# Optimization experiments

Hardware: AMD Instinct MI355X
Metric: run time of the kernel (lower is better)

Reference implementation:

```python
import jax, jax.numpy as jnp
import numpy as np

TAU = 2.0        # config.init_tau
VTH = 1.0        # config.v_threshold
KS = 25          # dilated_kernel_size == config.max_delay
EPS = 1e-5       # BatchNorm eps
ALPHA = 2.0      # atan surrogate alpha (spikingjelly default)

B, C_IN, C_INH, C_OUT, T, KC = 128, 512, 256, 512, 512, 1


def dcls_kernel(W, P, SIG):
    """Dcls1d 'gauss' version: build dense kernel [O, I, KS] by Gaussian
    interpolation of kernel_count weights at learnable positions P with
    spread SIG.  W, P, SIG: [O, I, KC]."""
    grid = jnp.arange(KS, dtype=W.dtype)                      # [KS]
    g = jnp.exp(-0.5 * ((grid - P[..., None]) / SIG[..., None]) ** 2)  # [O,I,KC,KS]
    g = g / (g.sum(-1, keepdims=True) + 1e-7)
    return jnp.einsum('oik,oikd->oid', W, g)                  # [O, I, KS]


def causal_conv1d(x, K):
    # x: [B, Cin, T], K: [Cout, Cin, KS] -> [B, Cout, T], left (causal) padding
    return jax.lax.conv_general_dilated(
        x, K, window_strides=(1,), padding=[(KS - 1, 0)],
        dimension_numbers=('NCH', 'OIH', 'NCH'))


@jax.custom_vjp
def spike_fn(v):
    return (v >= 0.0).astype(v.dtype)

def _spike_fwd(v):
    return spike_fn(v), v

def _spike_bwd(v, g):
    # atan surrogate gradient
    return (g * (ALPHA / 2.0) / (1.0 + (jnp.pi / 2.0 * ALPHA * v) ** 2),)

spike_fn.defvjp(_spike_fwd, _spike_bwd)


def lif_multistep(h):
    # h: [B, C, T] -> spikes [B, C, T]; decay_input=False, hard reset to 0,
    # detach_reset=True (stop_gradient on reset path)
    hT = jnp.transpose(h, (2, 0, 1))                          # [T, B, C]

    def step(v, h_t):
        v = v - v / TAU + h_t
        s = spike_fn(v - VTH)
        v = v * (1.0 - jax.lax.stop_gradient(s))
        return v, s

    v0 = jnp.zeros(hT.shape[1:], hT.dtype)
    _, sT = jax.lax.scan(step, v0, hT)
    return jnp.transpose(sT, (1, 2, 0))                       # [B, C, T]


def setup_inputs() -> dict:
    key = jax.random.key(0)
    ks = jax.random.split(key, 12)
    f = jnp.float32

    def w(k, o, i):
        return jax.random.uniform(k, (o, i, KC), dtype=f) / np.sqrt(i * KS)

    def p(k, o, i):
        return jax.random.uniform(k, (o, i, KC), dtype=f) * (KS - 1)

    return {
        'x': jax.random.normal(ks[0], (B, C_IN, T), dtype=f),
        'W_ie': w(ks[1], C_INH, C_IN), 'P_ie': p(ks[2], C_INH, C_IN),
        'SIG_ie': jnp.full((C_INH, C_IN, KC), 0.5, dtype=f),
        'W_oi': w(ks[3], C_OUT, C_INH), 'P_oi': p(ks[4], C_OUT, C_INH),
        'SIG_oi': jnp.full((C_OUT, C_INH, KC), 0.5, dtype=f),
        'W_ee': w(ks[5], C_OUT, C_IN), 'P_ee': p(ks[6], C_OUT, C_IN),
        'SIG_ee': jnp.full((C_OUT, C_IN, KC), 0.5, dtype=f),
        'bn_gamma': jnp.ones((C_INH,), dtype=f),
        'bn_beta': jnp.zeros((C_INH,), dtype=f),
        'bias': jax.random.uniform(ks[7], (C_OUT,), dtype=f,
                                   minval=-1.0, maxval=1.0) / np.sqrt(C_IN),
    }


def reference(x, W_ie, P_ie, SIG_ie, W_oi, P_oi, SIG_oi,
              W_ee, P_ee, SIG_ee, bn_gamma, bn_beta, bias):
    # input -> inhibitory (Dale positive weights)
    K_ie = dcls_kernel(jnp.abs(W_ie), P_ie, SIG_ie)
    h = causal_conv1d(x, K_ie)                                # [B, C_INH, T]

    # multi-step BatchNorm1d (training stats over batch and time)
    mean = h.mean((0, 2), keepdims=True)
    var = h.var((0, 2), keepdims=True)
    h = (h - mean) * jax.lax.rsqrt(var + EPS)
    h = h * bn_gamma[None, :, None] + bn_beta[None, :, None]

    # LIF spiking recurrence over time
    s = lif_multistep(h)                                      # [B, C_INH, T]

    # inhibitory -> output (Dale negative), input -> output (Dale positive)
    K_oi = dcls_kernel(-jnp.abs(W_oi), P_oi, SIG_oi)
    K_ee = dcls_kernel(jnp.abs(W_ee), P_ee, SIG_ee)
    out = causal_conv1d(s, K_oi) + causal_conv1d(x, K_ee)
    out = out + bias[None, :, None]
    return out
```

## Files before the change

### kernel.cpp

```cpp
#include <hip/hip_runtime.h>
#include <stdint.h>

#define B_    128
#define T_    512
#define PT_   536
#define CIN_  512
#define CINH_ 256
#define COUT_ 512
#define KS25  25

typedef __attribute__((ext_vector_type(8))) short s16x8;
typedef __attribute__((ext_vector_type(4))) float f32x4;

typedef const __attribute__((address_space(1))) void gas_t;
typedef __attribute__((address_space(3))) void las_t;

__device__ __forceinline__ short f2bf(float f) {
    union { float f; uint32_t u; } v; v.f = f;
    uint32_t r = v.u + 0x7fffu + ((v.u >> 16) & 1u);
    return (short)(r >> 16);
}
__device__ __forceinline__ float bf2f(short s) {
    union { uint32_t u; float f; } v; v.u = ((uint32_t)(uint16_t)s) << 16;
    return v.f;
}

__device__ __forceinline__ void gload16(const void* g, void* l) {
    __builtin_amdgcn_global_load_lds((gas_t*)g, (las_t*)l, 16, 0, 0);
}

template<int NCHUNK>
__device__ __forceinline__ void stage_tile(const short* src, short* lds, int stride, int tid) {
    const int wbase = tid & ~63;
    #pragma unroll
    for (int c = 0; c < (NCHUNK + 255) / 256; ++c) {
        int idx = c * 256 + tid;
        if ((NCHUNK % 256 == 0) || idx < NCHUNK) {
            int row = idx >> 3;
            int col = ((idx & 7) ^ (row & 7)) << 3;
            gload16(src + (size_t)row * stride + col, (char*)lds + (size_t)(c * 256 + wbase) * 16);
        }
    }
}

__device__ __forceinline__ void mfma_block(const short* Al, const short* Bl, int d,
                                           int wm, int wn, int l15, int kg, f32x4 acc[4][4]) {
    const int xa = (d + l15) & 7;
    const int xb = l15 & 7;
    #pragma unroll
    for (int kk = 0; kk < 2; ++kk) {
        const int ks = kk * 4 + kg;
        const int ka = (ks ^ xa) << 3;
        const int kb = (ks ^ xb) << 3;
        s16x8 a[4], b[4];
        #pragma unroll
        for (int m = 0; m < 4; ++m)
            a[m] = *(const s16x8*)(Al + (d + wm * 64 + m * 16 + l15) * 64 + ka);
        #pragma unroll
        for (int n = 0; n < 4; ++n)
            b[n] = *(const s16x8*)(Bl + (wn * 64 + n * 16 + l15) * 64 + kb);
        #pragma unroll
        for (int m = 0; m < 4; ++m)
            #pragma unroll
            for (int n = 0; n < 4; ++n)
                acc[m][n] = __builtin_amdgcn_mfma_f32_16x16x32_bf16(a[m], b[n], acc[m][n], 0, 0, 0);
    }
}

__device__ __forceinline__ void mfma_block3(const short* Ah, const short* Alo,
                                            const short* Bh, const short* Blo, int d,
                                            int wm, int wn, int l15, int kg, f32x4 acc[4][4]) {
    const int xa = (d + l15) & 7;
    const int xb = l15 & 7;
    #pragma unroll
    for (int kk = 0; kk < 2; ++kk) {
        const int ks = kk * 4 + kg;
        const int ka = (ks ^ xa) << 3;
        const int kb = (ks ^ xb) << 3;
        s16x8 ah[4], al[4], bh[4], bl[4];
        #pragma unroll
        for (int m = 0; m < 4; ++m) {
            const int ro = (d + wm * 64 + m * 16 + l15) * 64 + ka;
            ah[m] = *(const s16x8*)(Ah + ro);
            al[m] = *(const s16x8*)(Alo + ro);
        }
        #pragma unroll
        for (int n = 0; n < 4; ++n) {
            const int ro = (wn * 64 + n * 16 + l15) * 64 + kb;
            bh[n] = *(const s16x8*)(Bh + ro);
            bl[n] = *(const s16x8*)(Blo + ro);
        }
        #pragma unroll
        for (int m = 0; m < 4; ++m)
            #pragma unroll
            for (int n = 0; n < 4; ++n)
                acc[m][n] = __builtin_amdgcn_mfma_f32_16x16x32_bf16(ah[m], bh[n], acc[m][n], 0, 0, 0);
        #pragma unroll
        for (int m = 0; m < 4; ++m)
            #pragma unroll
            for (int n = 0; n < 4; ++n)
                acc[m][n] = __builtin_amdgcn_mfma_f32_16x16x32_bf16(ah[m], bl[n], acc[m][n], 0, 0, 0);
        #pragma unroll
        for (int m = 0; m < 4; ++m)
            #pragma unroll
            for (int n = 0; n < 4; ++n)
                acc[m][n] = __builtin_amdgcn_mfma_f32_16x16x32_bf16(al[m], bh[n], acc[m][n], 0, 0, 0);
    }
}


__global__ void zero_pads_kernel(short* xhi, short* xlo, short* sT, float* stats) {
    int idx = blockIdx.x * 256 + threadIdx.x;
    const int NX = B_ * 24 * CIN_;
    const int NS = B_ * 24 * CINH_;
    if (idx < NX) {
        int b = idx / (24 * CIN_), r = idx % (24 * CIN_);
        xhi[(size_t)b * PT_ * CIN_ + r] = 0;
        xlo[(size_t)b * PT_ * CIN_ + r] = 0;
    }
    if (idx < NS) {
        int b = idx / (24 * CINH_), r = idx % (24 * CINH_);
        sT[(size_t)b * PT_ * CINH_ + r] = 0;
    }
    if (idx < 512) stats[idx] = 0.f;
}

__global__ void build_k_kernel(const float* __restrict__ W, const float* __restrict__ P,
                               const float* __restrict__ SIG, short* __restrict__ K,
                               int O, int I, float sign) {
    int idx = blockIdx.x * 256 + threadIdx.x;
    if (idx >= O * I) return;
    float p = P[idx], sg = SIG[idx], w = fabsf(W[idx]) * sign;
    float g[KS25]; float s = 0.f;
    #pragma unroll
    for (int d = 0; d < KS25; ++d) { float z = ((float)d - p) / sg; float e = __expf(-0.5f * z * z); g[d] = e; s += e; }
    float inv = w / (s + 1e-7f);
    int OI = O * I;
    #pragma unroll
    for (int d = 0; d < KS25; ++d) K[(size_t)d * OI + idx] = f2bf(g[d] * inv);
}

__global__ void build_k_split_kernel(const float* __restrict__ W, const float* __restrict__ P,
                                     const float* __restrict__ SIG,
                                     short* __restrict__ Khi, short* __restrict__ Klo,
                                     int O, int I) {
    int idx = blockIdx.x * 256 + threadIdx.x;
    if (idx >= O * I) return;
    float p = P[idx], sg = SIG[idx], w = fabsf(W[idx]);
    float g[KS25]; float s = 0.f;
    #pragma unroll
    for (int d = 0; d < KS25; ++d) { float z = ((float)d - p) / sg; float e = __expf(-0.5f * z * z); g[d] = e; s += e; }
    float inv = w / (s + 1e-7f);
    int OI = O * I;
    #pragma unroll
    for (int d = 0; d < KS25; ++d) {
        float v = g[d] * inv;
        short hi = f2bf(v);
        Khi[(size_t)d * OI + idx] = hi;
        Klo[(size_t)d * OI + idx] = f2bf(v - bf2f(hi));
    }
}

__global__ void transpose_split_kernel(const float* __restrict__ x,
                                       short* __restrict__ xhi, short* __restrict__ xlo) {
    __shared__ float tile[32][33];
    int b = blockIdx.x, cb = blockIdx.y, tb = blockIdx.z;
    int tx = threadIdx.x, ty = threadIdx.y;
    #pragma unroll
    for (int r = 0; r < 4; ++r) {
        int c = cb * 32 + ty + r * 8;
        int t = tb * 32 + tx;
        tile[ty + r * 8][tx] = x[((size_t)b * CIN_ + c) * T_ + t];
    }
    __syncthreads();
    #pragma unroll
    for (int r = 0; r < 4; ++r) {
        int t = tb * 32 + ty + r * 8;
        int c = cb * 32 + tx;
        float v = tile[tx][ty + r * 8];
        short hi = f2bf(v);
        size_t o = ((size_t)b * PT_ + 24 + t) * CIN_ + c;
        xhi[o] = hi;
        xlo[o] = f2bf(v - bf2f(hi));
    }
}

__global__ void bn_stats_kernel(const float* __restrict__ h, float* __restrict__ stats) {
    int c = threadIdx.x;
    int r0 = blockIdx.x * 128;
    float s = 0.f, s2 = 0.f;
    for (int r = 0; r < 128; ++r) {
        float v = h[(size_t)(r0 + r) * CINH_ + c];
        s += v; s2 += v * v;
    }
    atomicAdd(&stats[c], s);
    atomicAdd(&stats[256 + c], s2);
}

__global__ void bn_final_kernel(const float* __restrict__ stats, const float* __restrict__ gamma,
                                const float* __restrict__ beta, float* __restrict__ bnp) {
    int c = threadIdx.x;
    const float invN = 1.f / (float)(B_ * T_);
    float mean = stats[c] * invN;
    float var = stats[256 + c] * invN - mean * mean;
    float sc = gamma[c] * rsqrtf(var + 1e-5f);
    bnp[c] = sc;
    bnp[256 + c] = beta[c] - mean * sc;
}

__global__ __launch_bounds__(64) void lif_kernel(const float* __restrict__ h,
                                                 const float* __restrict__ bnp,
                                                 short* __restrict__ sT) {
    int bidx = blockIdx.x;
    int b = bidx >> 2;
    int c = (bidx & 3) * 64 + threadIdx.x;
    float sc = bnp[c], sh = bnp[256 + c];
    const float* hp = h + (size_t)b * T_ * CINH_ + c;
    short* sp = sT + ((size_t)b * PT_ + 24) * CINH_ + c;
    float v = 0.f;
    #pragma unroll 4
    for (int t = 0; t < T_; ++t) {
        float hv = hp[(size_t)t * CINH_] * sc + sh;
        v = 0.5f * v + hv;
        bool spike = (v >= 1.0f);
        sp[(size_t)t * CINH_] = spike ? (short)0x3F80 : (short)0;
        v = spike ? 0.f : v;
    }
}


__global__ __launch_bounds__(256, 2)
void conv_ie_kernel(const short* __restrict__ xhi, const short* __restrict__ xlo,
                    const short* __restrict__ Khi, const short* __restrict__ Klo,
                    float* __restrict__ h) {
    __shared__ short Ah[152 * 64], Alo[152 * 64], Bh[128 * 64], Blo[128 * 64];
    const int tid = threadIdx.x;
    const int wave = tid >> 6, lane = tid & 63;
    const int wm = wave >> 1, wn = wave & 1;
    const int l15 = lane & 15, kg = lane >> 4;
    const int bid = blockIdx.x;
    const int nt = bid & 1, mt = bid >> 1;
    const int b = mt >> 2, t0 = (mt & 3) << 7;
    const int o0 = nt << 7;

    f32x4 acc[4][4];
    const f32x4 zero = {0.f, 0.f, 0.f, 0.f};
    #pragma unroll
    for (int m = 0; m < 4; ++m)
        #pragma unroll
        for (int n = 0; n < 4; ++n) acc[m][n] = zero;

    const short* A0h = xhi + ((size_t)b * PT_ + t0) * CIN_;
    const short* A0l = xlo + ((size_t)b * PT_ + t0) * CIN_;
    const short* K0h = Khi + (size_t)o0 * CIN_;
    const short* K0l = Klo + (size_t)o0 * CIN_;

    #pragma unroll 1
    for (int ci0 = 0; ci0 < CIN_; ci0 += 64) {
        stage_tile<1216>(A0h + ci0, Ah, CIN_, tid);
        stage_tile<1216>(A0l + ci0, Alo, CIN_, tid);
        #pragma unroll 1
        for (int d = 0; d < KS25; ++d) {
            stage_tile<1024>(K0h + (size_t)d * CINH_ * CIN_ + ci0, Bh, CIN_, tid);
            stage_tile<1024>(K0l + (size_t)d * CINH_ * CIN_ + ci0, Blo, CIN_, tid);
            __syncthreads();
            mfma_block3(Ah, Alo, Bh, Blo, d, wm, wn, l15, kg, acc);
            __syncthreads();
        }
    }
    #pragma unroll
    for (int m = 0; m < 4; ++m) {
        const int trb = t0 + wm * 64 + m * 16 + kg * 4;
        #pragma unroll
        for (int n = 0; n < 4; ++n) {
            const int c = o0 + wn * 64 + n * 16 + l15;
            f32x4 v = acc[m][n];
            h[((size_t)b * T_ + trb + 0) * CINH_ + c] = v.x;
            h[((size_t)b * T_ + trb + 1) * CINH_ + c] = v.y;
            h[((size_t)b * T_ + trb + 2) * CINH_ + c] = v.z;
            h[((size_t)b * T_ + trb + 3) * CINH_ + c] = v.w;
        }
    }
}

__global__ __launch_bounds__(256, 2)
void conv_out_kernel(const short* __restrict__ xT, const short* __restrict__ sT,
                     const short* __restrict__ Kee, const short* __restrict__ Koi,
                     const float* __restrict__ bias, float* __restrict__ out) {
    __shared__ short Al[152 * 64];
    __shared__ short Bl[128 * 64];
    const int tid = threadIdx.x;
    const int wave = tid >> 6, lane = tid & 63;
    const int wm = wave >> 1, wn = wave & 1;
    const int l15 = lane & 15, kg = lane >> 4;
    const int bid = blockIdx.x;
    const int nt = bid & 3, mt = bid >> 2;
    const int b = mt >> 2, t0 = (mt & 3) << 7;
    const int o0 = nt << 7;

    f32x4 acc[4][4];
    const f32x4 zero = {0.f, 0.f, 0.f, 0.f};
    #pragma unroll
    for (int m = 0; m < 4; ++m)
        #pragma unroll
        for (int n = 0; n < 4; ++n) acc[m][n] = zero;

    {
        const short* A0 = xT + ((size_t)b * PT_ + t0) * CIN_;
        const short* K0 = Kee + (size_t)o0 * CIN_;
        #pragma unroll 1
        for (int ci0 = 0; ci0 < CIN_; ci0 += 64) {
            stage_tile<1216>(A0 + ci0, Al, CIN_, tid);
            #pragma unroll 1
            for (int d = 0; d < KS25; ++d) {
                stage_tile<1024>(K0 + (size_t)d * COUT_ * CIN_ + ci0, Bl, CIN_, tid);
                __syncthreads();
                mfma_block(Al, Bl, d, wm, wn, l15, kg, acc);
                __syncthreads();
            }
        }
    }
    {
        const short* A0 = sT + ((size_t)b * PT_ + t0) * CINH_;
        const short* K0 = Koi + (size_t)o0 * CINH_;
        #pragma unroll 1
        for (int ci0 = 0; ci0 < CINH_; ci0 += 64) {
            stage_tile<1216>(A0 + ci0, Al, CINH_, tid);
            #pragma unroll 1
            for (int d = 0; d < KS25; ++d) {
                stage_tile<1024>(K0 + (size_t)d * COUT_ * CINH_ + ci0, Bl, CINH_, tid);
                __syncthreads();
                mfma_block(Al, Bl, d, wm, wn, l15, kg, acc);
                __syncthreads();
            }
        }
    }
    #pragma unroll
    for (int n = 0; n < 4; ++n) {
        const int o = o0 + wn * 64 + n * 16 + l15;
        const float bv = bias[o];
        #pragma unroll
        for (int m = 0; m < 4; ++m) {
            const int tr = t0 + wm * 64 + m * 16 + kg * 4;
            f32x4 v = acc[m][n];
            v.x += bv; v.y += bv; v.z += bv; v.w += bv;
            *(f32x4*)&out[((size_t)b * COUT_ + o) * T_ + tr] = v;
        }
    }
}


extern "C" void kernel_launch(void* const* d_in, const int* in_sizes, int n_in,
                              void* d_out, int out_size, void* d_ws, size_t ws_size,
                              hipStream_t stream) {
    const float* x     = (const float*)d_in[0];
    const float* W_ie  = (const float*)d_in[1];
    const float* P_ie  = (const float*)d_in[2];
    const float* S_ie  = (const float*)d_in[3];
    const float* W_oi  = (const float*)d_in[4];
    const float* P_oi  = (const float*)d_in[5];
    const float* S_oi  = (const float*)d_in[6];
    const float* W_ee  = (const float*)d_in[7];
    const float* P_ee  = (const float*)d_in[8];
    const float* S_ee  = (const float*)d_in[9];
    const float* gamma = (const float*)d_in[10];
    const float* beta  = (const float*)d_in[11];
    const float* bias  = (const float*)d_in[12];
    float* out = (float*)d_out;

    char* w = (char*)d_ws;
    size_t off = 0;
    auto take = [&](size_t n) { char* p = w + off; off += (n + 255) & ~(size_t)255; return p; };

    short* xhi   = (short*)take((size_t)B_ * PT_ * CIN_ * 2);
    short* xlo   = (short*)take((size_t)B_ * PT_ * CIN_ * 2);
    short* sT    = (short*)take((size_t)B_ * PT_ * CINH_ * 2);
    short* Kie_h = (short*)take((size_t)KS25 * CINH_ * CIN_ * 2);
    short* Kie_l = (short*)take((size_t)KS25 * CINH_ * CIN_ * 2);
    short* Koi   = (short*)take((size_t)KS25 * COUT_ * CINH_ * 2);
    short* Kee   = (short*)take((size_t)KS25 * COUT_ * CIN_ * 2);
    float* h     = (float*)take((size_t)B_ * T_ * CINH_ * 4);
    float* stats = (float*)take(512 * 4);
    float* bnp   = (float*)take(512 * 4);

    zero_pads_kernel<<<6144, 256, 0, stream>>>(xhi, xlo, sT, stats);
    build_k_split_kernel<<<(CINH_ * CIN_ + 255) / 256, 256, 0, stream>>>(W_ie, P_ie, S_ie, Kie_h, Kie_l, CINH_, CIN_);
    build_k_kernel<<<(COUT_ * CINH_ + 255) / 256, 256, 0, stream>>>(W_oi, P_oi, S_oi, Koi, COUT_, CINH_, -1.f);
    build_k_kernel<<<(COUT_ * CIN_ + 255) / 256, 256, 0, stream>>>(W_ee, P_ee, S_ee, Kee, COUT_, CIN_, 1.f);
    transpose_split_kernel<<<dim3(B_, CIN_ / 32, T_ / 32), dim3(32, 8), 0, stream>>>(x, xhi, xlo);
    conv_ie_kernel<<<(B_ * T_ / 128) * (CINH_ / 128), 256, 0, stream>>>(xhi, xlo, Kie_h, Kie_l, h);
    bn_stats_kernel<<<512, 256, 0, stream>>>(h, stats);
    bn_final_kernel<<<1, 256, 0, stream>>>(stats, gamma, beta, bnp);
    lif_kernel<<<B_ * (CINH_ / 64), 64, 0, stream>>>(h, bnp, sT);
    conv_out_kernel<<<(B_ * T_ / 128) * (COUT_ / 128), 256, 0, stream>>>(xhi, sT, Kee, Koi, bias, out);
}
```

Before: 2.055 ms.

## Double-buffer kernel-weight tiles and shrink conv_ie output tile to 64 channels

Both conv kernels now double-buffer the weight (B) tile in shared memory. The next delay tap's tile is staged while MFMAs run on the current one, which removes one of the two barriers per tap. conv_ie now uses a 128x64 output tile with twice as many blocks, presumably to fit the extra LDS and reduce register pressure, and its three split-precision MFMAs are interleaved per fragment. conv_out's occupancy hint goes from 2 to 3 blocks, which risks spilling its 4x4 accumulators, and the doubled B buffer raises its LDS use.

```diff
diff --git a/kernel.cpp b/kernel.cpp
--- a/kernel.cpp
+++ b/kernel.cpp
@@ -69,7 +69,7 @@
 
 __device__ __forceinline__ void mfma_block3(const short* Ah, const short* Alo,
                                             const short* Bh, const short* Blo, int d,
-                                            int wm, int wn, int l15, int kg, f32x4 acc[4][4]) {
+                                            int wm, int wn, int l15, int kg, f32x4 acc[4][2]) {
     const int xa = (d + l15) & 7;
     const int xb = l15 & 7;
     #pragma unroll
@@ -77,7 +77,7 @@
         const int ks = kk * 4 + kg;
         const int ka = (ks ^ xa) << 3;
         const int kb = (ks ^ xb) << 3;
-        s16x8 ah[4], al[4], bh[4], bl[4];
+        s16x8 ah[4], al[4], bh[2], bl[2];
         #pragma unroll
         for (int m = 0; m < 4; ++m) {
             const int ro = (d + wm * 64 + m * 16 + l15) * 64 + ka;
@@ -85,26 +85,19 @@
             al[m] = *(const s16x8*)(Alo + ro);
         }
         #pragma unroll
-        for (int n = 0; n < 4; ++n) {
-            const int ro = (wn * 64 + n * 16 + l15) * 64 + kb;
+        for (int n = 0; n < 2; ++n) {
+            const int ro = (wn * 32 + n * 16 + l15) * 64 + kb;
             bh[n] = *(const s16x8*)(Bh + ro);
             bl[n] = *(const s16x8*)(Blo + ro);
         }
         #pragma unroll
         for (int m = 0; m < 4; ++m)
             #pragma unroll
-            for (int n = 0; n < 4; ++n)
+            for (int n = 0; n < 2; ++n) {
                 acc[m][n] = __builtin_amdgcn_mfma_f32_16x16x32_bf16(ah[m], bh[n], acc[m][n], 0, 0, 0);
-        #pragma unroll
-        for (int m = 0; m < 4; ++m)
-            #pragma unroll
-            for (int n = 0; n < 4; ++n)
                 acc[m][n] = __builtin_amdgcn_mfma_f32_16x16x32_bf16(ah[m], bl[n], acc[m][n], 0, 0, 0);
-        #pragma unroll
-        for (int m = 0; m < 4; ++m)
-            #pragma unroll
-            for (int n = 0; n < 4; ++n)
                 acc[m][n] = __builtin_amdgcn_mfma_f32_16x16x32_bf16(al[m], bh[n], acc[m][n], 0, 0, 0);
+            }
     }
 }
 
@@ -233,47 +226,55 @@
 void conv_ie_kernel(const short* __restrict__ xhi, const short* __restrict__ xlo,
                     const short* __restrict__ Khi, const short* __restrict__ Klo,
                     float* __restrict__ h) {
-    __shared__ short Ah[152 * 64], Alo[152 * 64], Bh[128 * 64], Blo[128 * 64];
+    __shared__ short Ah[152 * 64], Alo[152 * 64];
+    __shared__ short Bh[2][64 * 64], Blo[2][64 * 64];
     const int tid = threadIdx.x;
     const int wave = tid >> 6, lane = tid & 63;
     const int wm = wave >> 1, wn = wave & 1;
     const int l15 = lane & 15, kg = lane >> 4;
     const int bid = blockIdx.x;
-    const int nt = bid & 1, mt = bid >> 1;
+    const int nt = bid & 3, mt = bid >> 2;
     const int b = mt >> 2, t0 = (mt & 3) << 7;
-    const int o0 = nt << 7;
-
-    f32x4 acc[4][4];
+    const int o0 = nt << 6;
+
+    f32x4 acc[4][2];
     const f32x4 zero = {0.f, 0.f, 0.f, 0.f};
     #pragma unroll
     for (int m = 0; m < 4; ++m)
         #pragma unroll
-        for (int n = 0; n < 4; ++n) acc[m][n] = zero;
+        for (int n = 0; n < 2; ++n) acc[m][n] = zero;
 
     const short* A0h = xhi + ((size_t)b * PT_ + t0) * CIN_;
     const short* A0l = xlo + ((size_t)b * PT_ + t0) * CIN_;
     const short* K0h = Khi + (size_t)o0 * CIN_;
     const short* K0l = Klo + (size_t)o0 * CIN_;
-
+    const size_t dstride = (size_t)CINH_ * CIN_;
+
+    int buf = 0;
     #pragma unroll 1
     for (int ci0 = 0; ci0 < CIN_; ci0 += 64) {
         stage_tile<1216>(A0h + ci0, Ah, CIN_, tid);
         stage_tile<1216>(A0l + ci0, Alo, CIN_, tid);
+        stage_tile<512>(K0h + ci0, Bh[buf], CIN_, tid);
+        stage_tile<512>(K0l + ci0, Blo[buf], CIN_, tid);
+        __syncthreads();
         #pragma unroll 1
         for (int d = 0; d < KS25; ++d) {
-            stage_tile<1024>(K0h + (size_t)d * CINH_ * CIN_ + ci0, Bh, CIN_, tid);
-            stage_tile<1024>(K0l + (size_t)d * CINH_ * CIN_ + ci0, Blo, CIN_, tid);
+            if (d + 1 < KS25) {
+                stage_tile<512>(K0h + (size_t)(d + 1) * dstride + ci0, Bh[buf ^ 1], CIN_, tid);
+                stage_tile<512>(K0l + (size_t)(d + 1) * dstride + ci0, Blo[buf ^ 1], CIN_, tid);
+            }
+            mfma_block3(Ah, Alo, Bh[buf], Blo[buf], d, wm, wn, l15, kg, acc);
             __syncthreads();
-            mfma_block3(Ah, Alo, Bh, Blo, d, wm, wn, l15, kg, acc);
-            __syncthreads();
+            buf ^= 1;
         }
     }
     #pragma unroll
     for (int m = 0; m < 4; ++m) {
         const int trb = t0 + wm * 64 + m * 16 + kg * 4;
         #pragma unroll
-        for (int n = 0; n < 4; ++n) {
-            const int c = o0 + wn * 64 + n * 16 + l15;
+        for (int n = 0; n < 2; ++n) {
+            const int c = o0 + wn * 32 + n * 16 + l15;
             f32x4 v = acc[m][n];
             h[((size_t)b * T_ + trb + 0) * CINH_ + c] = v.x;
             h[((size_t)b * T_ + trb + 1) * CINH_ + c] = v.y;
@@ -283,12 +284,12 @@
     }
 }
 
-__global__ __launch_bounds__(256, 2)
+__global__ __launch_bounds__(256, 3)
 void conv_out_kernel(const short* __restrict__ xT, const short* __restrict__ sT,
                      const short* __restrict__ Kee, const short* __restrict__ Koi,
                      const float* __restrict__ bias, float* __restrict__ out) {
     __shared__ short Al[152 * 64];
-    __shared__ short Bl[128 * 64];
+    __shared__ short Bl[2][128 * 64];
     const int tid = threadIdx.x;
     const int wave = tid >> 6, lane = tid & 63;
     const int wm = wave >> 1, wn = wave & 1;
@@ -305,33 +306,42 @@
         #pragma unroll
         for (int n = 0; n < 4; ++n) acc[m][n] = zero;
 
+    int buf = 0;
     {
         const short* A0 = xT + ((size_t)b * PT_ + t0) * CIN_;
         const short* K0 = Kee + (size_t)o0 * CIN_;
+        const size_t dstride = (size_t)COUT_ * CIN_;
         #pragma unroll 1
         for (int ci0 = 0; ci0 < CIN_; ci0 += 64) {
             stage_tile<1216>(A0 + ci0, Al, CIN_, tid);
+            stage_tile<1024>(K0 + ci0, Bl[buf], CIN_, tid);
+            __syncthreads();
             #pragma unroll 1
             for (int d = 0; d < KS25; ++d) {
-                stage_tile<1024>(K0 + (size_t)d * COUT_ * CIN_ + ci0, Bl, CIN_, tid);
+                if (d + 1 < KS25)
+                    stage_tile<1024>(K0 + (size_t)(d + 1) * dstride + ci0, Bl[buf ^ 1], CIN_, tid);
+                mfma_block(Al, Bl[buf], d, wm, wn, l15, kg, acc);
                 __syncthreads();
-                mfma_block(Al, Bl, d, wm, wn, l15, kg, acc);
-                __syncthreads();
+                buf ^= 1;
             }
         }
     }
     {
         const short* A0 = sT + ((size_t)b * PT_ + t0) * CINH_;
         const short* K0 = Koi + (size_t)o0 * CINH_;
+        const size_t dstride = (size_t)COUT_ * CINH_;
         #pragma unroll 1
         for (int ci0 = 0; ci0 < CINH_; ci0 += 64) {
             stage_tile<1216>(A0 + ci0, Al, CINH_, tid);
+            stage_tile<1024>(K0 + ci0, Bl[buf], CINH_, tid);
+            __syncthreads();
             #pragma unroll 1
             for (int d = 0; d < KS25; ++d) {
-                stage_tile<1024>(K0 + (size_t)d * COUT_ * CINH_ + ci0, Bl, CINH_, tid);
+                if (d + 1 < KS25)
+                    stage_tile<1024>(K0 + (size_t)(d + 1) * dstride + ci0, Bl[buf ^ 1], CINH_, tid);
+                mfma_block(Al, Bl[buf], d, wm, wn, l15, kg, acc);
                 __syncthreads();
-                mfma_block(Al, Bl, d, wm, wn, l15, kg, acc);
-                __syncthreads();
+                buf ^= 1;
             }
         }
     }
@@ -388,7 +398,7 @@
     build_k_kernel<<<(COUT_ * CINH_ + 255) / 256, 256, 0, stream>>>(W_oi, P_oi, S_oi, Koi, COUT_, CINH_, -1.f);
     build_k_kernel<<<(COUT_ * CIN_ + 255) / 256, 256, 0, stream>>>(W_ee, P_ee, S_ee, Kee, COUT_, CIN_, 1.f);
     transpose_split_kernel<<<dim3(B_, CIN_ / 32, T_ / 32), dim3(32, 8), 0, stream>>>(x, xhi, xlo);
-    conv_ie_kernel<<<(B_ * T_ / 128) * (CINH_ / 128), 256, 0, stream>>>(xhi, xlo, Kie_h, Kie_l, h);
+    conv_ie_kernel<<<(B_ * T_ / 128) * (CINH_ / 64), 256, 0, stream>>>(xhi, xlo, Kie_h, Kie_l, h);
     bn_stats_kernel<<<512, 256, 0, stream>>>(h, stats);
     bn_final_kernel<<<1, 256, 0, stream>>>(stats, gamma, beta, bnp);
     lif_kernel<<<B_ * (CINH_ / 64), 64, 0, stream>>>(h, bnp, sT);
```

Result: slower. 2.183 ms (+6.3%).
